# Optimization experiments

Measured on AMD Instinct MI355X. Metric: run time of the kernel, lower is better.

The kernel has to match this reference:

```python
import jax, jax.numpy as jnp
import numpy as np

B, T, H, W = 4, 8, 14, 14
IN_DIMS = 768
OUT_DIMS = 768
HEADS = 12
HD = OUT_DIMS // HEADS  # 64
N = T * H * W + 1  # 1569 tokens incl. cls
SCALE = HD ** -0.5
EPS = 1e-5


def _ln(x, w, b):
    m = jnp.mean(x, -1, keepdims=True)
    v = jnp.mean((x - m) ** 2, -1, keepdims=True)
    return (x - m) * jax.lax.rsqrt(v + EPS) * w + b


def _pool(t, conv_w, nw, nb, Tq, Hq, Wq):
    # t: (B, heads, N, C) with leading cls token. Depthwise 3x3x3 conv, stride 1, pad 1.
    Bn, Hn, _, C = t.shape
    cls_tok, sp = t[:, :, :1], t[:, :, 1:]
    xc = sp.reshape(Bn * Hn, Tq, Hq, Wq, C).transpose(0, 4, 1, 2, 3)  # (B*h, C, T, H, W)
    xc = jax.lax.conv_general_dilated(
        xc, conv_w, (1, 1, 1), [(1, 1)] * 3,
        dimension_numbers=('NCDHW', 'OIDHW', 'NCDHW'), feature_group_count=C)
    xc = xc.reshape(Bn, Hn, C, Tq * Hq * Wq).swapaxes(2, 3)  # (B, h, L, C)
    xc = jnp.concatenate([cls_tok, xc], axis=2)
    return _ln(xc, nw, nb)


def _rel_lookup(rel, q_size, k_size):
    # stride_q == stride_kv == 1 -> q_size == k_size and rel already has 2*size-1 rows,
    # so no interpolation / ratio scaling is needed.
    coords = jnp.arange(q_size)[:, None] - jnp.arange(k_size)[None, :] + (k_size - 1)
    return rel[coords]  # (q, k, C)


def setup_inputs():
    key = jax.random.key(0)
    ks = jax.random.split(key, 12)
    w = lambda i, shape: jax.random.normal(ks[i], shape, jnp.float32) * 0.02
    return {
        'x': jax.random.normal(ks[0], (B, N, IN_DIMS), jnp.float32),
        'qkv_w': w(1, (IN_DIMS, 3 * OUT_DIMS)),
        'qkv_b': jnp.zeros((3 * OUT_DIMS,), jnp.float32),
        'proj_w': w(2, (OUT_DIMS, OUT_DIMS)),
        'proj_b': jnp.zeros((OUT_DIMS,), jnp.float32),
        'pool_q_w': w(3, (HD, 1, 3, 3, 3)),
        'pool_k_w': w(4, (HD, 1, 3, 3, 3)),
        'pool_v_w': w(5, (HD, 1, 3, 3, 3)),
        'norm_q_w': jnp.ones((HD,), jnp.float32), 'norm_q_b': jnp.zeros((HD,), jnp.float32),
        'norm_k_w': jnp.ones((HD,), jnp.float32), 'norm_k_b': jnp.zeros((HD,), jnp.float32),
        'norm_v_w': jnp.ones((HD,), jnp.float32), 'norm_v_b': jnp.zeros((HD,), jnp.float32),
        'rel_pos_t': w(6, (2 * T - 1, HD)),
        'rel_pos_h': w(7, (2 * H - 1, HD)),
        'rel_pos_w': w(8, (2 * W - 1, HD)),
        't_size': T, 'h_size': H, 'w_size': W,
    }


def reference(x, qkv_w, qkv_b, proj_w, proj_b, pool_q_w, pool_k_w, pool_v_w,
              norm_q_w, norm_q_b, norm_k_w, norm_k_b, norm_v_w, norm_v_b,
              rel_pos_t, rel_pos_h, rel_pos_w, t_size, h_size, w_size):
    Bn, Nn, _ = x.shape
    qkv = (x @ qkv_w + qkv_b).reshape(Bn, Nn, 3, HEADS, HD)
    qkv = jnp.transpose(qkv, (2, 0, 3, 1, 4))  # (3, B, heads, N, HD)
    q, k, v = qkv[0], qkv[1], qkv[2]
    q = _pool(q, pool_q_w, norm_q_w, norm_q_b, t_size, h_size, w_size)
    k = _pool(k, pool_k_w, norm_k_w, norm_k_b, t_size, h_size, w_size)
    v = _pool(v, pool_v_w, norm_v_w, norm_v_b, t_size, h_size, w_size)
    attn = jnp.einsum('bhqc,bhkc->bhqk', q * SCALE, k)
    # Decomposed spatiotemporal relative position bias on the non-cls block.
    Rt = _rel_lookup(rel_pos_t, t_size, t_size)
    Rh = _rel_lookup(rel_pos_h, h_size, h_size)
    Rw = _rel_lookup(rel_pos_w, w_size, w_size)
    r_q = q[:, :, 1:].reshape(Bn, HEADS, t_size, h_size, w_size, HD)
    rel_t = jnp.einsum('bythwc,tkc->bythwk', r_q, Rt)
    rel_h = jnp.einsum('bythwc,hkc->bythwk', r_q, Rh)
    rel_w = jnp.einsum('bythwc,wkc->bythwk', r_q, Rw)
    bias = (rel_t[..., :, None, None] + rel_h[..., None, :, None]
            + rel_w[..., None, None, :])  # (B, h, qt, qh, qw, kt, kh, kw)
    L = t_size * h_size * w_size
    attn = attn.at[:, :, 1:, 1:].add(bias.reshape(Bn, HEADS, L, L))
    attn = jax.nn.softmax(attn, axis=-1)
    out = jnp.einsum('bhqk,bhkc->bhqc', attn, v)
    out = out.at[:, :, 1:, :].add(q[:, :, 1:, :])  # residual pooling (cls excluded)
    out = out.swapaxes(1, 2).reshape(Bn, Nn, OUT_DIMS)
    return out @ proj_w + proj_b
```

## Files before the change

### kernel.cpp

```cpp
#include <hip/hip_runtime.h>
#include <cstdint>
#include <cstddef>

typedef __attribute__((ext_vector_type(8))) short short8;
typedef __attribute__((ext_vector_type(4))) short short4v;
typedef __attribute__((ext_vector_type(4))) float f32x4;
typedef unsigned short u16;

#define DI __device__ __forceinline__

constexpr int BATCH = 4;
constexpr int HEADS = 12, HD = 64;
constexpr int NTOK = 1569;
constexpr int NPAD = 1600;
constexpr int QPAD = 1664;
constexpr int DIM = 768, DIM3 = 2304;
constexpr int MROWS = BATCH * NTOK;
constexpr int MP = 6400;
constexpr int AUG = 128;
constexpr int BHN = BATCH * HEADS;
constexpr float LOG2E = 1.4426950408889634f;
constexpr float QSCALE = 0.125f * LOG2E;
constexpr float RESID = 8.0f / LOG2E;
constexpr float LN_EPS = 1e-5f;

DI u16 f2bf(float x) {
  union { float f; unsigned u; } v; v.f = x;
  unsigned r = v.u + 0x7FFFu + ((v.u >> 16) & 1u);
  return (u16)(r >> 16);
}
DI float bf2f(u16 h) {
  union { unsigned u; float f; } v; v.u = ((unsigned)h) << 16;
  return v.f;
}

typedef const __attribute__((address_space(1))) unsigned int gu32;
typedef __attribute__((address_space(3))) unsigned int lu32;
DI void gld16(const void* g, void* l) {
  __builtin_amdgcn_global_load_lds((gu32*)g, (lu32*)l, 16, 0, 0);
}

__global__ __launch_bounds__(256) void k_cast_x(const float* __restrict__ x,
                                                u16* __restrict__ xb) {
  int i = (blockIdx.x * 256 + threadIdx.x) * 4;
  if (i >= MP * DIM) return;
  int row = i / DIM;
  short4v o;
  if (row < MROWS) {
    float4 v = *(const float4*)(x + i);
    o.x = (short)f2bf(v.x); o.y = (short)f2bf(v.y);
    o.z = (short)f2bf(v.z); o.w = (short)f2bf(v.w);
  } else {
    o.x = 0; o.y = 0; o.z = 0; o.w = 0;
  }
  *(short4v*)(xb + i) = o;
}

__global__ __launch_bounds__(256) void k_transpose_cast(const float* __restrict__ src,
                                                        u16* __restrict__ dst,
                                                        int K, int NC) {
  __shared__ float tile[32][33];
  const int ntiles = NC >> 5;
  const int bx = blockIdx.x % ntiles;
  const int by = blockIdx.x / ntiles;
  const int tx = threadIdx.x & 31, ty = threadIdx.x >> 5;
  const int n0 = bx * 32, k0 = by * 32;
#pragma unroll
  for (int r = 0; r < 32; r += 8)
    tile[ty + r][tx] = src[(size_t)(k0 + ty + r) * NC + n0 + tx];
  __syncthreads();
#pragma unroll
  for (int r = 0; r < 32; r += 8)
    dst[(size_t)(n0 + ty + r) * K + k0 + tx] = f2bf(tile[tx][ty + r]);
}

template <int EPI>
__global__ __launch_bounds__(256) void k_gemm(const u16* __restrict__ A,
                                              const u16* __restrict__ Bt,
                                              const float* __restrict__ bias,
                                              float* __restrict__ out) {
  __shared__ __align__(16) u16 sA[128 * 64];
  __shared__ __align__(16) u16 sB[128 * 64];
  const int tid = threadIdx.x;
  const int w = tid >> 6, lane = tid & 63;
  const int g = lane >> 4, lr = lane & 15;
  const int brow = blockIdx.x * 128, bcol = blockIdx.y * 128;
  const int wr = w >> 1, wc = w & 1;

  f32x4 acc[4][4];
#pragma unroll
  for (int m = 0; m < 4; ++m)
#pragma unroll
    for (int n = 0; n < 4; ++n) {
      acc[m][n].x = 0.f; acc[m][n].y = 0.f; acc[m][n].z = 0.f; acc[m][n].w = 0.f;
    }

  for (int kt = 0; kt < 12; ++kt) {
    __syncthreads();
#pragma unroll
    for (int j = 0; j < 4; ++j) {
      int cb = (j * 4 + w) * 64;
      int chunk = cb + lane;
      int row = chunk >> 3, ch = chunk & 7;
      int gch = ch ^ (row & 7);
      gld16(A + (size_t)(brow + row) * DIM + kt * 64 + gch * 8, &sA[cb * 8]);
      gld16(Bt + (size_t)(bcol + row) * DIM + kt * 64 + gch * 8, &sB[cb * 8]);
    }
    __syncthreads();

    short8 af[4][2], bfr[4][2];
#pragma unroll
    for (int m = 0; m < 4; ++m) {
      int row = wr * 64 + m * 16 + lr;
      int sw = row & 7;
#pragma unroll
      for (int ks = 0; ks < 2; ++ks)
        af[m][ks] = *(const short8*)&sA[row * 64 + (((ks * 4 + g) ^ sw) * 8)];
    }
#pragma unroll
    for (int n = 0; n < 4; ++n) {
      int row = wc * 64 + n * 16 + lr;
      int sw = row & 7;
#pragma unroll
      for (int ks = 0; ks < 2; ++ks)
        bfr[n][ks] = *(const short8*)&sB[row * 64 + (((ks * 4 + g) ^ sw) * 8)];
    }
#pragma unroll
    for (int m = 0; m < 4; ++m)
#pragma unroll
      for (int n = 0; n < 4; ++n) {
        acc[m][n] = __builtin_amdgcn_mfma_f32_16x16x32_bf16(af[m][0], bfr[n][0], acc[m][n], 0, 0, 0);
        acc[m][n] = __builtin_amdgcn_mfma_f32_16x16x32_bf16(af[m][1], bfr[n][1], acc[m][n], 0, 0, 0);
      }
  }

#pragma unroll
  for (int m = 0; m < 4; ++m)
#pragma unroll
    for (int n = 0; n < 4; ++n) {
      int gj = bcol + wc * 64 + n * 16 + lr;
      float bv = bias[gj];
#pragma unroll
      for (int r = 0; r < 4; ++r) {
        int gm = brow + wr * 64 + m * 16 + g * 4 + r;
        if (gm >= MROWS) continue;
        float v = acc[m][n][r] + bv;
        if (EPI == 0) {
          int t = gj >= 1536 ? 2 : (gj >= 768 ? 1 : 0);
          int rem = gj - t * 768;
          int h = rem >> 6, c = rem & 63;
          int b = gm >= 3 * NTOK ? 3 : (gm >= 2 * NTOK ? 2 : (gm >= NTOK ? 1 : 0));
          int nt = gm - b * NTOK;
          out[(((size_t)(t * BATCH + b) * HEADS + h) * NPAD + nt) * HD + c] = v;
        } else {
          out[(size_t)gm * DIM + gj] = v;
        }
      }
    }
}

DI float ldsrc(const float* __restrict__ src, int tt, int h2, int w2, int lane) {
  if ((unsigned)tt >= 8u || (unsigned)h2 >= 14u || (unsigned)w2 >= 14u) return 0.f;
  return src[(size_t)(1 + (tt * 14 + h2) * 14 + w2) * HD + lane];
}

__global__ __launch_bounds__(256, 4) void k_pool(
    const float* __restrict__ qkv,
    const float* __restrict__ pw_q, const float* __restrict__ pw_k, const float* __restrict__ pw_v,
    const float* __restrict__ nw_q, const float* __restrict__ nb_q,
    const float* __restrict__ nw_k, const float* __restrict__ nb_k,
    const float* __restrict__ nw_v, const float* __restrict__ nb_v,
    u16* __restrict__ Qa, u16* __restrict__ Ka, u16* __restrict__ Vt) {
  const int wv = threadIdx.x >> 6, lane = threadIdx.x & 63;
  const int unit = blockIdx.x % 29;
  const int taubh = blockIdx.x / 29;
  const int tau = taubh / BHN, bh = taubh % BHN;
  const float* src = qkv + ((size_t)tau * BHN + bh) * ((size_t)NPAD * HD);
  const float* nw = tau == 0 ? nw_q : tau == 1 ? nw_k : nw_v;
  const float* nb = tau == 0 ? nb_q : tau == 1 ? nb_k : nb_v;

  if (unit == 28) {
    if (wv == 0) {
      float val = src[lane];
      float s = val, sq = val * val;
#pragma unroll
      for (int off = 1; off < 64; off <<= 1) { s += __shfl_xor(s, off); sq += __shfl_xor(sq, off); }
      float mean = s * (1.f / 64.f);
      float var = sq * (1.f / 64.f) - mean * mean;
      float ln = (val - mean) * rsqrtf(var + LN_EPS) * nw[lane] + nb[lane];
      if (tau == 0)      { size_t base = (size_t)bh * QPAD * AUG; Qa[base + lane] = f2bf(ln * QSCALE); Qa[base + 64 + lane] = 0; }
      else if (tau == 1) { size_t base = (size_t)bh * NPAD * AUG; Ka[base + lane] = f2bf(ln); Ka[base + 64 + lane] = 0; }
      else               { Vt[((size_t)bh * HD + lane) * NPAD] = f2bf(ln); }
    } else {
      int lim = (tau == 0) ? QPAD : NPAD;
      for (int n = 1569 + (wv - 1); n < lim; n += 3) {
        if (tau == 0) {
          size_t base = ((size_t)bh * QPAD + n) * AUG;
          Qa[base + lane] = 0; Qa[base + 64 + lane] = 0;
        } else if (tau == 1) {
          size_t base = ((size_t)bh * NPAD + n) * AUG;
          Ka[base + lane] = 0; Ka[base + 64 + lane] = 0;
        } else {
          Vt[((size_t)bh * HD + lane) * NPAD + n] = 0;
        }
      }
    }
    return;
  }

  const int th = unit * 4 + wv;
  const int t = th / 14, hh = th % 14;

  float wt[27];
  {
    const float* wp = (tau == 0 ? pw_q : tau == 1 ? pw_k : pw_v) + lane * 27;
#pragma unroll
    for (int j = 0; j < 27; ++j) wt[j] = wp[j];
  }

  float win[9][3];
#pragma unroll
  for (int dt = 0; dt < 3; ++dt)
#pragma unroll
    for (int dh = 0; dh < 3; ++dh) {
      win[dt * 3 + dh][0] = 0.f;
      win[dt * 3 + dh][1] = ldsrc(src, t + dt - 1, hh + dh - 1, 0, lane);
      win[dt * 3 + dh][2] = ldsrc(src, t + dt - 1, hh + dh - 1, 1, lane);
    }

#pragma unroll
  for (int ww = 0; ww < 14; ++ww) {
    float nxt[9];
#pragma unroll
    for (int dt = 0; dt < 3; ++dt)
#pragma unroll
      for (int dh = 0; dh < 3; ++dh)
        nxt[dt * 3 + dh] = ldsrc(src, t + dt - 1, hh + dh - 1, ww + 2, lane);

    float a = 0.f;
#pragma unroll
    for (int i = 0; i < 9; ++i)
      a += win[i][0] * wt[i * 3 + 0] + win[i][1] * wt[i * 3 + 1] + win[i][2] * wt[i * 3 + 2];

    float s = a, sq = a * a;
#pragma unroll
    for (int off = 1; off < 64; off <<= 1) { s += __shfl_xor(s, off); sq += __shfl_xor(sq, off); }
    float mean = s * (1.f / 64.f);
    float var = sq * (1.f / 64.f) - mean * mean;
    float ln = (a - mean) * rsqrtf(var + LN_EPS) * nw[lane] + nb[lane];

    const int n = 1 + (t * 14 + hh) * 14 + ww;
    if (tau == 0) {
      size_t base = ((size_t)bh * QPAD + n) * AUG;
      Qa[base + lane] = f2bf(ln * QSCALE);
      Qa[base + 64 + lane] = 0;
    } else if (tau == 1) {
      size_t base = ((size_t)bh * NPAD + n) * AUG;
      Ka[base + lane] = f2bf(ln);
      u16 e = 0;
      if (lane == t || lane == 8 + hh || lane == 22 + ww) e = 0x3F80;
      Ka[base + 64 + lane] = e;
    } else {
      Vt[((size_t)bh * HD + lane) * NPAD + n] = f2bf(ln);
    }

#pragma unroll
    for (int i = 0; i < 9; ++i) { win[i][0] = win[i][1]; win[i][1] = win[i][2]; win[i][2] = nxt[i]; }
  }
}

__global__ __launch_bounds__(256) void k_rel(const float* __restrict__ rel_t,
                                             const float* __restrict__ rel_h,
                                             const float* __restrict__ rel_w,
                                             u16* __restrict__ Qa) {
  __shared__ __align__(16) u16 sR[80 * 72];
  const int tid = threadIdx.x, w = tid >> 6, lane = tid & 63;
  const int g = lane >> 4, lr = lane & 15;
  const int bh = blockIdx.x / 25, qt = blockIdx.x % 25;

  for (int idx = tid; idx < 80 * 64; idx += 256) {
    int j = idx >> 6, c = idx & 63;
    float v = 0.f;
    if (j < 15)      v = rel_t[j * HD + c];
    else if (j < 42) v = rel_h[(j - 15) * HD + c];
    else if (j < 69) v = rel_w[(j - 42) * HD + c];
    sR[j * 72 + c] = f2bf(v * 8.f);
  }
  __syncthreads();

  const int q0 = qt * 64 + w * 16;
  short8 aq[2];
  {
    const u16* qrow = Qa + ((size_t)bh * QPAD + q0 + lr) * AUG;
    aq[0] = *(const short8*)(qrow + g * 8);
    aq[1] = *(const short8*)(qrow + 32 + g * 8);
  }

  f32x4 acc[5];
#pragma unroll
  for (int jt = 0; jt < 5; ++jt) {
    f32x4 a; a.x = 0.f; a.y = 0.f; a.z = 0.f; a.w = 0.f;
    int row = jt * 16 + lr;
    short8 b0 = *(const short8*)&sR[row * 72 + g * 8];
    short8 b1 = *(const short8*)&sR[row * 72 + (4 + g) * 8];
    a = __builtin_amdgcn_mfma_f32_16x16x32_bf16(aq[0], b0, a, 0, 0, 0);
    a = __builtin_amdgcn_mfma_f32_16x16x32_bf16(aq[1], b1, a, 0, 0, 0);
    acc[jt] = a;
  }

#pragma unroll
  for (int jt = 0; jt < 5; ++jt) {
    int j = jt * 16 + lr;
#pragma unroll
    for (int r = 0; r < 4; ++r) {
      int gq = q0 + g * 4 + r;
      if (gq < 1 || gq >= NTOK) continue;
      int p = gq - 1;
      int t = p / 196, pr = p - t * 196;
      int hh = pr / 14, ww = pr - hh * 14;
      int it = t + 7 - j;
      int ih = hh + 28 - j;
      int iw = ww + 55 - j;
      int i = -1;
      if ((unsigned)it < 8u) i = it;
      else if ((unsigned)ih < 14u) i = 8 + ih;
      else if ((unsigned)iw < 14u) i = 22 + iw;
      if (i >= 0)
        Qa[((size_t)bh * QPAD + gq) * AUG + 64 + i] = f2bf(acc[jt][r]);
    }
  }
}

__global__ __launch_bounds__(256, 3) void k_attn(const u16* __restrict__ Qa,
                                                 const u16* __restrict__ Ka,
                                                 const u16* __restrict__ Vt,
                                                 u16* __restrict__ Opart,
                                                 float* __restrict__ lsum) {
  __shared__ __align__(16) u16 sK[64 * 128];
  __shared__ __align__(16) u16 sV[2][64 * 64];
  __shared__ __align__(16) u16 sP[4][32 * 72];
  const int tid = threadIdx.x, w = tid >> 6, lane = tid & 63;
  const int g = lane >> 4, lr = lane & 15;
  const int bid = blockIdx.x;
  const int swz = (bid & 7) * 156 + (bid >> 3);
  const int bh = swz / 26, rem2 = swz % 26;
  const int half = rem2 / 13, qt = rem2 % 13;
  const int qw = qt * 128 + w * 32;
  const int kb0 = half * 13;
  const int kbN = half ? 12 : 13;

  short8 aq[2][4];
#pragma unroll
  for (int f = 0; f < 2; ++f) {
    const u16* qrow = Qa + ((size_t)bh * QPAD + qw + f * 16 + lr) * AUG;
#pragma unroll
    for (int ks = 0; ks < 4; ++ks) aq[f][ks] = *(const short8*)(qrow + ks * 32 + g * 8);
  }

  short8 vones;
#pragma unroll
  for (int i = 0; i < 8; ++i) vones[i] = (short)0x3F80;

  const u16* kgp[4];
  u16* kld[4];
#pragma unroll
  for (int j = 0; j < 4; ++j) {
    int idx = j * 256 + tid;
    int row = idx >> 4, ch = idx & 15;
    int gch = ch ^ (row & 7);
    kgp[j] = Ka + ((size_t)bh * NPAD + kb0 * 64 + row) * AUG + gch * 8;
    kld[j] = &sK[(j * 256 + w * 64) * 8];
  }
  const u16* vgp[2];
  int vld[2];
#pragma unroll
  for (int j = 0; j < 2; ++j) {
    int idx = j * 256 + tid;
    int row = idx >> 3, ch = idx & 7;
    int gch = ch ^ (row & 7);
    vgp[j] = Vt + ((size_t)bh * HD + row) * NPAD + kb0 * 64 + gch * 8;
    vld[j] = (j * 256 + w * 64) * 8;
  }

#pragma unroll
  for (int j = 0; j < 4; ++j) { gld16(kgp[j], kld[j]); kgp[j] += 64 * AUG; }
#pragma unroll
  for (int j = 0; j < 2; ++j) { gld16(vgp[j], &sV[0][vld[j]]); vgp[j] += 64; }
  __syncthreads();

  f32x4 O[2][5];
#pragma unroll
  for (int f = 0; f < 2; ++f)
#pragma unroll
    for (int c4 = 0; c4 < 5; ++c4) { O[f][c4].x = 0.f; O[f][c4].y = 0.f; O[f][c4].z = 0.f; O[f][c4].w = 0.f; }

  int cur = 0;
  for (int it = 0; it < kbN; ++it) {
    f32x4 sacc[2][4];
    __builtin_amdgcn_s_setprio(1);
#pragma unroll
    for (int ct = 0; ct < 4; ++ct) {
      int row = ct * 16 + lr;
      int sw = row & 7;
      short8 bk[4];
#pragma unroll
      for (int ks = 0; ks < 4; ++ks)
        bk[ks] = *(const short8*)&sK[row * 128 + (((ks * 4 + g) ^ sw) << 3)];
#pragma unroll
      for (int f = 0; f < 2; ++f) {
        f32x4 a; a.x = 0.f; a.y = 0.f; a.z = 0.f; a.w = 0.f;
#pragma unroll
        for (int ks = 0; ks < 4; ++ks)
          a = __builtin_amdgcn_mfma_f32_16x16x32_bf16(bk[ks], aq[f][ks], a, 0, 0, 0);
        sacc[f][ct] = a;
      }
    }
    __builtin_amdgcn_s_setprio(0);
    __syncthreads();

    if (it + 1 < kbN) {
#pragma unroll
      for (int j = 0; j < 4; ++j) { gld16(kgp[j], kld[j]); kgp[j] += 64 * AUG; }
#pragma unroll
      for (int j = 0; j < 2; ++j) { gld16(vgp[j], &sV[cur ^ 1][vld[j]]); vgp[j] += 64; }
    }

    if (kb0 + it == 24) {
#pragma unroll
      for (int f = 0; f < 2; ++f) {
        sacc[f][2][0] = (g == 0) ? sacc[f][2][0] : -1e30f;
        sacc[f][2][1] = -1e30f; sacc[f][2][2] = -1e30f; sacc[f][2][3] = -1e30f;
        sacc[f][3][0] = -1e30f; sacc[f][3][1] = -1e30f;
        sacc[f][3][2] = -1e30f; sacc[f][3][3] = -1e30f;
      }
    }

#pragma unroll
    for (int f = 0; f < 2; ++f) {
      int ro = (f * 16 + lr) * 72;
#pragma unroll
      for (int ct = 0; ct < 4; ++ct) {
        unsigned u0 = __float_as_uint(exp2f(sacc[f][ct][0]));
        unsigned u1 = __float_as_uint(exp2f(sacc[f][ct][1]));
        unsigned u2 = __float_as_uint(exp2f(sacc[f][ct][2]));
        unsigned u3 = __float_as_uint(exp2f(sacc[f][ct][3]));
        uint2 pk;
        pk.x = __builtin_amdgcn_perm(u1, u0, 0x07060302u);
        pk.y = __builtin_amdgcn_perm(u3, u2, 0x07060302u);
        *(uint2*)&sP[w][ro + ct * 16 + g * 4] = pk;
      }
    }

    __builtin_amdgcn_s_setprio(1);
#pragma unroll
    for (int kk = 0; kk < 2; ++kk) {
      short8 ap[2];
#pragma unroll
      for (int f = 0; f < 2; ++f)
        ap[f] = *(const short8*)&sP[w][(f * 16 + lr) * 72 + kk * 32 + g * 8];
#pragma unroll
      for (int c4 = 0; c4 < 4; ++c4) {
        int row = c4 * 16 + lr;
        int sw = row & 7;
        short8 bv = *(const short8*)&sV[cur][row * 64 + (((kk * 4 + g) ^ sw) << 3)];
#pragma unroll
        for (int f = 0; f < 2; ++f)
          O[f][c4] = __builtin_amdgcn_mfma_f32_16x16x32_bf16(ap[f], bv, O[f][c4], 0, 0, 0);
      }
#pragma unroll
      for (int f = 0; f < 2; ++f)
        O[f][4] = __builtin_amdgcn_mfma_f32_16x16x32_bf16(ap[f], vones, O[f][4], 0, 0, 0);
    }
    __builtin_amdgcn_s_setprio(0);

    __syncthreads();
    cur ^= 1;
  }

  size_t pbase = (size_t)(bh * 2 + half) * QPAD;
#pragma unroll
  for (int f = 0; f < 2; ++f)
#pragma unroll
    for (int r = 0; r < 4; ++r) {
      int qg = qw + f * 16 + g * 4 + r;
      if (qg >= NTOK) continue;
      float l = O[f][4][r];
      float inv = 1.f / l;
#pragma unroll
      for (int c4 = 0; c4 < 4; ++c4)
        Opart[(pbase + qg) * 64 + c4 * 16 + lr] = f2bf(O[f][c4][r] * inv);
      if (lr == 0) lsum[pbase + qg] = l;
    }
}

__global__ __launch_bounds__(256) void k_comb(const u16* __restrict__ Opart,
                                              const float* __restrict__ lsum,
                                              const u16* __restrict__ Qa,
                                              u16* __restrict__ outA) {
  const int wv = threadIdx.x >> 6, lane = threadIdx.x & 63;
  int rid = blockIdx.x * 4 + wv;
  if (rid >= BHN * NTOK) return;
  int bh = rid / NTOK, qg = rid - bh * NTOK;
  size_t base0 = (size_t)(bh * 2) * QPAD + qg;
  size_t base1 = base0 + QPAD;
  float l0 = lsum[base0], l1 = lsum[base1];
  float inv = 1.f / (l0 + l1);
  float o0 = bf2f(Opart[base0 * 64 + lane]);
  float o1 = bf2f(Opart[base1 * 64 + lane]);
  float v = (l0 * o0 + l1 * o1) * inv;
  if (qg >= 1) v += RESID * bf2f(Qa[((size_t)bh * QPAD + qg) * AUG + lane]);
  int b = bh / HEADS, h = bh - b * HEADS;
  outA[((size_t)(b * NTOK + qg)) * DIM + h * HD + lane] = f2bf(v);
}

extern "C" void kernel_launch(void* const* d_in, const int* in_sizes, int n_in,
                              void* d_out, int out_size, void* d_ws, size_t ws_size,
                              hipStream_t stream) {
  (void)in_sizes; (void)n_in; (void)out_size; (void)ws_size;
  const float* x      = (const float*)d_in[0];
  const float* qkv_w  = (const float*)d_in[1];
  const float* qkv_b  = (const float*)d_in[2];
  const float* proj_w = (const float*)d_in[3];
  const float* proj_b = (const float*)d_in[4];
  const float* pw_q   = (const float*)d_in[5];
  const float* pw_k   = (const float*)d_in[6];
  const float* pw_v   = (const float*)d_in[7];
  const float* nw_q   = (const float*)d_in[8];
  const float* nb_q   = (const float*)d_in[9];
  const float* nw_k   = (const float*)d_in[10];
  const float* nb_k   = (const float*)d_in[11];
  const float* nw_v   = (const float*)d_in[12];
  const float* nb_v   = (const float*)d_in[13];
  const float* rel_t  = (const float*)d_in[14];
  const float* rel_h  = (const float*)d_in[15];
  const float* rel_w  = (const float*)d_in[16];
  float* out = (float*)d_out;

  char* ws = (char*)d_ws;
  size_t off = 0;
  auto alloc = [&](size_t bytes) -> void* {
    off = (off + 511) & ~(size_t)511;
    void* p = ws + off;
    off += bytes;
    return p;
  };
  u16*   xb     = (u16*)alloc((size_t)MP * DIM * 2);
  u16*   qkvwT  = (u16*)alloc((size_t)DIM3 * DIM * 2);
  u16*   projwT = (u16*)alloc((size_t)DIM * DIM * 2);
  float* qkvf   = (float*)alloc((size_t)3 * BHN * NPAD * HD * 4);
  u16*   Qa     = (u16*)alloc((size_t)BHN * QPAD * AUG * 2);
  u16*   Ka     = (u16*)alloc((size_t)BHN * NPAD * AUG * 2);
  u16*   Vt     = (u16*)alloc((size_t)BHN * HD * NPAD * 2);
  u16*   attnO  = (u16*)alloc((size_t)MP * DIM * 2);
  u16*   Opart  = (u16*)alloc((size_t)BHN * 2 * QPAD * HD * 2);
  float* lbuf   = (float*)alloc((size_t)BHN * 2 * QPAD * 4);

  k_cast_x<<<dim3(MP * DIM / 1024), dim3(256), 0, stream>>>(x, xb);
  k_transpose_cast<<<dim3((DIM3 / 32) * (DIM / 32)), dim3(256), 0, stream>>>(qkv_w, qkvwT, DIM, DIM3);
  k_transpose_cast<<<dim3((DIM / 32) * (DIM / 32)), dim3(256), 0, stream>>>(proj_w, projwT, DIM, DIM);

  k_gemm<0><<<dim3(MP / 128, DIM3 / 128), dim3(256), 0, stream>>>(xb, qkvwT, qkv_b, qkvf);

  k_pool<<<dim3(3 * BHN * 29), dim3(256), 0, stream>>>(
      qkvf, pw_q, pw_k, pw_v, nw_q, nb_q, nw_k, nb_k, nw_v, nb_v,
      Qa, Ka, Vt);

  k_rel<<<dim3(BHN * 25), dim3(256), 0, stream>>>(rel_t, rel_h, rel_w, Qa);

  k_attn<<<dim3(BHN * 26), dim3(256), 0, stream>>>(Qa, Ka, Vt, Opart, lbuf);

  k_comb<<<dim3((BHN * NTOK + 3) / 4), dim3(256), 0, stream>>>(Opart, lbuf, Qa, attnO);

  k_gemm<1><<<dim3(MP / 128, DIM / 128), dim3(256), 0, stream>>>(attnO, projwT, proj_b, out);
}
```

Before: 248.2 us.

## Store QKV intermediate as bf16 and streamline pooling loads and reductions

The QKV GEMM now writes its head-split output as bf16 instead of fp32, halving the intermediate buffer's write and read traffic. The pooling kernel reads bf16 and swaps out-of-range boundary checks for precomputed row offsets that point at a zeroed pad region, which a memset clears. Wave reductions use DPP row shifts plus two shuffles, and the launch bound asks for higher occupancy. Rounding the pre-conv activations to bf16 adds some precision loss.

```diff
diff --git a/kernel.cpp b/kernel.cpp
--- a/kernel.cpp
+++ b/kernel.cpp
@@ -23,6 +23,7 @@
 constexpr float QSCALE = 0.125f * LOG2E;
 constexpr float RESID = 8.0f / LOG2E;
 constexpr float LN_EPS = 1e-5f;
+constexpr int SLAB = NPAD * HD;
 
 DI u16 f2bf(float x) {
   union { float f; unsigned u; } v; v.f = x;
@@ -38,6 +39,21 @@
 typedef __attribute__((address_space(3))) unsigned int lu32;
 DI void gld16(const void* g, void* l) {
   __builtin_amdgcn_global_load_lds((gu32*)g, (lu32*)l, 16, 0, 0);
+}
+
+DI float redsum64(float x) {
+  int t;
+  t = __builtin_amdgcn_update_dpp(__float_as_int(x), __float_as_int(x), 0x121, 0xF, 0xF, false);
+  x += __int_as_float(t);
+  t = __builtin_amdgcn_update_dpp(__float_as_int(x), __float_as_int(x), 0x122, 0xF, 0xF, false);
+  x += __int_as_float(t);
+  t = __builtin_amdgcn_update_dpp(__float_as_int(x), __float_as_int(x), 0x124, 0xF, 0xF, false);
+  x += __int_as_float(t);
+  t = __builtin_amdgcn_update_dpp(__float_as_int(x), __float_as_int(x), 0x128, 0xF, 0xF, false);
+  x += __int_as_float(t);
+  x += __shfl_xor(x, 16);
+  x += __shfl_xor(x, 32);
+  return x;
 }
 
 __global__ __launch_bounds__(256) void k_cast_x(const float* __restrict__ x,
@@ -78,7 +94,7 @@
 __global__ __launch_bounds__(256) void k_gemm(const u16* __restrict__ A,
                                               const u16* __restrict__ Bt,
                                               const float* __restrict__ bias,
-                                              float* __restrict__ out) {
+                                              void* __restrict__ outv) {
   __shared__ __align__(16) u16 sA[128 * 64];
   __shared__ __align__(16) u16 sB[128 * 64];
   const int tid = threadIdx.x;
@@ -151,21 +167,16 @@
           int h = rem >> 6, c = rem & 63;
           int b = gm >= 3 * NTOK ? 3 : (gm >= 2 * NTOK ? 2 : (gm >= NTOK ? 1 : 0));
           int nt = gm - b * NTOK;
-          out[(((size_t)(t * BATCH + b) * HEADS + h) * NPAD + nt) * HD + c] = v;
+          ((u16*)outv)[(((size_t)(t * BATCH + b) * HEADS + h) * NPAD + nt) * HD + c] = f2bf(v);
         } else {
-          out[(size_t)gm * DIM + gj] = v;
+          ((float*)outv)[(size_t)gm * DIM + gj] = v;
         }
       }
     }
 }
 
-DI float ldsrc(const float* __restrict__ src, int tt, int h2, int w2, int lane) {
-  if ((unsigned)tt >= 8u || (unsigned)h2 >= 14u || (unsigned)w2 >= 14u) return 0.f;
-  return src[(size_t)(1 + (tt * 14 + h2) * 14 + w2) * HD + lane];
-}
-
-__global__ __launch_bounds__(256, 4) void k_pool(
-    const float* __restrict__ qkv,
+__global__ __launch_bounds__(256, 6) void k_pool(
+    const u16* __restrict__ qkv,
     const float* __restrict__ pw_q, const float* __restrict__ pw_k, const float* __restrict__ pw_v,
     const float* __restrict__ nw_q, const float* __restrict__ nb_q,
     const float* __restrict__ nw_k, const float* __restrict__ nb_k,
@@ -175,16 +186,16 @@
   const int unit = blockIdx.x % 29;
   const int taubh = blockIdx.x / 29;
   const int tau = taubh / BHN, bh = taubh % BHN;
-  const float* src = qkv + ((size_t)tau * BHN + bh) * ((size_t)NPAD * HD);
+  const u16* src = qkv + (size_t)taubh * SLAB;
+  const int zoff = (3 * BHN - taubh) * SLAB;
   const float* nw = tau == 0 ? nw_q : tau == 1 ? nw_k : nw_v;
   const float* nb = tau == 0 ? nb_q : tau == 1 ? nb_k : nb_v;
 
   if (unit == 28) {
     if (wv == 0) {
-      float val = src[lane];
-      float s = val, sq = val * val;
-#pragma unroll
-      for (int off = 1; off < 64; off <<= 1) { s += __shfl_xor(s, off); sq += __shfl_xor(sq, off); }
+      float val = bf2f(src[lane]);
+      float s = redsum64(val);
+      float sq = redsum64(val * val);
       float mean = s * (1.f / 64.f);
       float var = sq * (1.f / 64.f) - mean * mean;
       float ln = (val - mean) * rsqrtf(var + LN_EPS) * nw[lane] + nb[lane];
@@ -218,33 +229,38 @@
     for (int j = 0; j < 27; ++j) wt[j] = wp[j];
   }
 
+  int roff[9];
+#pragma unroll
+  for (int dt = 0; dt < 3; ++dt)
+#pragma unroll
+    for (int dh = 0; dh < 3; ++dh) {
+      int tt = t + dt - 1, h2 = hh + dh - 1;
+      bool ok = ((unsigned)tt < 8u) && ((unsigned)h2 < 14u);
+      roff[dt * 3 + dh] = (ok ? (1 + (tt * 14 + h2) * 14) * HD : zoff) + lane;
+    }
+
   float win[9][3];
 #pragma unroll
-  for (int dt = 0; dt < 3; ++dt)
-#pragma unroll
-    for (int dh = 0; dh < 3; ++dh) {
-      win[dt * 3 + dh][0] = 0.f;
-      win[dt * 3 + dh][1] = ldsrc(src, t + dt - 1, hh + dh - 1, 0, lane);
-      win[dt * 3 + dh][2] = ldsrc(src, t + dt - 1, hh + dh - 1, 1, lane);
-    }
+  for (int i = 0; i < 9; ++i) {
+    win[i][0] = 0.f;
+    win[i][1] = bf2f(src[roff[i]]);
+    win[i][2] = bf2f(src[roff[i] + HD]);
+  }
 
 #pragma unroll
   for (int ww = 0; ww < 14; ++ww) {
     float nxt[9];
 #pragma unroll
-    for (int dt = 0; dt < 3; ++dt)
-#pragma unroll
-      for (int dh = 0; dh < 3; ++dh)
-        nxt[dt * 3 + dh] = ldsrc(src, t + dt - 1, hh + dh - 1, ww + 2, lane);
+    for (int i = 0; i < 9; ++i)
+      nxt[i] = (ww + 2 < 14) ? bf2f(src[roff[i] + (ww + 2) * HD]) : 0.f;
 
     float a = 0.f;
 #pragma unroll
     for (int i = 0; i < 9; ++i)
       a += win[i][0] * wt[i * 3 + 0] + win[i][1] * wt[i * 3 + 1] + win[i][2] * wt[i * 3 + 2];
 
-    float s = a, sq = a * a;
-#pragma unroll
-    for (int off = 1; off < 64; off <<= 1) { s += __shfl_xor(s, off); sq += __shfl_xor(sq, off); }
+    float s = redsum64(a);
+    float sq = redsum64(a * a);
     float mean = s * (1.f / 64.f);
     float var = sq * (1.f / 64.f) - mean * mean;
     float ln = (a - mean) * rsqrtf(var + LN_EPS) * nw[lane] + nb[lane];
@@ -547,7 +563,7 @@
   u16*   xb     = (u16*)alloc((size_t)MP * DIM * 2);
   u16*   qkvwT  = (u16*)alloc((size_t)DIM3 * DIM * 2);
   u16*   projwT = (u16*)alloc((size_t)DIM * DIM * 2);
-  float* qkvf   = (float*)alloc((size_t)3 * BHN * NPAD * HD * 4);
+  u16*   qkvf   = (u16*)alloc((size_t)3 * BHN * SLAB * 2 + 2048);
   u16*   Qa     = (u16*)alloc((size_t)BHN * QPAD * AUG * 2);
   u16*   Ka     = (u16*)alloc((size_t)BHN * NPAD * AUG * 2);
   u16*   Vt     = (u16*)alloc((size_t)BHN * HD * NPAD * 2);
@@ -555,6 +571,8 @@
   u16*   Opart  = (u16*)alloc((size_t)BHN * 2 * QPAD * HD * 2);
   float* lbuf   = (float*)alloc((size_t)BHN * 2 * QPAD * 4);
 
+  hipMemsetAsync(qkvf + (size_t)3 * BHN * SLAB, 0, 2048, stream);
+
   k_cast_x<<<dim3(MP * DIM / 1024), dim3(256), 0, stream>>>(x, xb);
   k_transpose_cast<<<dim3((DIM3 / 32) * (DIM / 32)), dim3(256), 0, stream>>>(qkv_w, qkvwT, DIM, DIM3);
   k_transpose_cast<<<dim3((DIM / 32) * (DIM / 32)), dim3(256), 0, stream>>>(proj_w, projwT, DIM, DIM);
```

Measured after the change: 295.3 us. +19.0%, slower.
